# Kernel optimization log

Hardware: AMD Instinct MI355X
Metric: run time of the kernel (lower is better)

The kernel has to match this reference:

```python
import jax, jax.numpy as jnp
import numpy as np

N = 50000   # nodes
E = 1000000 # edges
D = 64      # input_dim
H = 64      # hidden dim (both hidden layers)
O = 16      # output_dim
G = 512     # number of graphs in the batch


def setup_inputs() -> dict:
    key = jax.random.key(0)
    ks = jax.random.split(key, 12)
    s = 0.05
    x = jax.random.normal(ks[0], (N, D), dtype=jnp.float32)
    edge_index = jax.random.randint(ks[1], (2, E), 0, N, dtype=jnp.int32)
    batch = jnp.sort(jax.random.randint(ks[2], (N,), 0, G, dtype=jnp.int32))
    # SAGEConv layer 1: lin_l (neighbor aggregate, with bias), lin_r (root, no bias)
    Wl1 = jax.random.normal(ks[3], (D, H), dtype=jnp.float32) * s
    Wr1 = jax.random.normal(ks[4], (D, H), dtype=jnp.float32) * s
    b1 = jnp.zeros((H,), dtype=jnp.float32)
    # SAGEConv layer 2
    Wl2 = jax.random.normal(ks[5], (H, H), dtype=jnp.float32) * s
    Wr2 = jax.random.normal(ks[6], (H, H), dtype=jnp.float32) * s
    b2 = jnp.zeros((H,), dtype=jnp.float32)
    # final Linear head
    Wo = jax.random.normal(ks[7], (H, O), dtype=jnp.float32) * s
    bo = jnp.zeros((O,), dtype=jnp.float32)
    return {"x": x, "edge_index": edge_index, "batch": batch,
            "Wl1": Wl1, "Wr1": Wr1, "b1": b1,
            "Wl2": Wl2, "Wr2": Wr2, "b2": b2,
            "Wo": Wo, "bo": bo}


def reference(x, edge_index, batch, Wl1, Wr1, b1, Wl2, Wr2, b2, Wo, bo):
    src, dst = edge_index[0], edge_index[1]  # source_to_target message flow

    def sage(h, Wl, Wr, b):
        # aggr='add': sum messages x_j from src into dst, then
        # out = lin_l(aggr) + lin_r(h)   (PyG SAGEConv, bias on lin_l)
        agg = jax.ops.segment_sum(h[src], dst, num_segments=N)  # [N, d]
        return agg @ Wl + h @ Wr + b

    h = jax.nn.relu(sage(x, Wl1, Wr1, b1))
    h = jax.nn.relu(sage(h, Wl2, Wr2, b2))
    g = jax.ops.segment_sum(h, batch, num_segments=G)  # global_add_pool -> [G, H]
    # dropout is identity in eval mode
    return g @ Wo + bo  # [G, O]
```

## Files before the change

kernel.cpp:

```cpp
#include <hip/hip_runtime.h>


namespace {
constexpr int NN = 50000;
constexpr int NE = 1000000;
constexpr int NG = 512;
constexpr int NO = 16;
constexpr int KB = 98;
constexpr int BCAP = 16000;
constexpr int EPT = 8;
constexpr int EPB = 256 * EPT;
constexpr int SBLK = (NE + EPB - 1) / EPB;
constexpr int SEDGE = 12288;
constexpr int CVT_BLK = (NN * 64 / 8 + 255) / 256;
constexpr int WP_BLK = 64;
}

typedef __attribute__((ext_vector_type(8))) short bf16x8;
typedef __attribute__((ext_vector_type(4))) float f32x4;

__device__ __forceinline__ unsigned short f2bf(float f) {
  unsigned u = __float_as_uint(f);
  u += 0x7FFFu + ((u >> 16) & 1u);
  return (unsigned short)(u >> 16);
}

__global__ __launch_bounds__(256) void prep_all(
    const float* __restrict__ x, unsigned short* __restrict__ x_bf,
    const float* __restrict__ Wl1, const float* __restrict__ Wr1,
    const float* __restrict__ Wl2, const float* __restrict__ Wr2,
    unsigned short* __restrict__ Wt1, unsigned short* __restrict__ Wt2,
    const int* __restrict__ ei, int* __restrict__ bcount,
    unsigned int* __restrict__ ebuf) {
  __shared__ unsigned int stage[EPB];
  __shared__ int cnt[128];
  __shared__ int lbase[128];
  __shared__ int cur[128];
  __shared__ int gbase[128];
  __shared__ int total_sh;
  int b = blockIdx.x;
  int t = threadIdx.x;

  if (b < CVT_BLK) {
    int i = b * 256 + t;
    if (i >= NN * 8) return;
    const float4* p = reinterpret_cast<const float4*>(x) + (size_t)i * 2;
    float4 a = p[0], bb = p[1];
    uint4 u;
    u.x = (unsigned)f2bf(a.x) | ((unsigned)f2bf(a.y) << 16);
    u.y = (unsigned)f2bf(a.z) | ((unsigned)f2bf(a.w) << 16);
    u.z = (unsigned)f2bf(bb.x) | ((unsigned)f2bf(bb.y) << 16);
    u.w = (unsigned)f2bf(bb.z) | ((unsigned)f2bf(bb.w) << 16);
    reinterpret_cast<uint4*>(x_bf)[i] = u;
    return;
  }
  if (b < CVT_BLK + WP_BLK) {
    int id = (b - CVT_BLK) * 256 + t;
    int half = id >> 13;
    int e = id & 8191;
    int nrow = e >> 7;
    int kk = e & 127;
    const float* Wl = half ? Wl2 : Wl1;
    const float* Wr = half ? Wr2 : Wr1;
    unsigned short* Wt = half ? Wt2 : Wt1;
    float v = (kk < 64) ? Wl[kk * 64 + nrow] : Wr[(kk - 64) * 64 + nrow];
    Wt[nrow * 128 + kk] = f2bf(v);
    return;
  }
  int sb = b - (CVT_BLK + WP_BLK);
  if (t < 128) cnt[t] = 0;
  __syncthreads();
  int e0 = sb * EPB;
  unsigned int pk[EPT];
#pragma unroll
  for (int i = 0; i < EPT; ++i) {
    int e = e0 + i * 256 + t;
    if (e < NE) {
      unsigned int src = (unsigned int)ei[e];
      unsigned int dst = (unsigned int)ei[NE + e];
      pk[i] = (dst << 16) | src;
      atomicAdd(&cnt[dst >> 9], 1);
    } else {
      pk[i] = 0xFFFFFFFFu;
    }
  }
  __syncthreads();
  int deg = (t < 128) ? cnt[t] : 0;
  for (int off = 1; off < 128; off <<= 1) {
    int u = (t >= off && t < 128) ? cnt[t - off] : 0;
    __syncthreads();
    if (t < 128) cnt[t] += u;
    __syncthreads();
  }
  if (t < 128) {
    int excl = cnt[t] - deg;
    lbase[t] = excl;
    cur[t] = excl;
    if (t < KB) gbase[t] = t * BCAP + atomicAdd(&bcount[t], deg);
    if (t == 127) total_sh = cnt[127];
  }
  __syncthreads();
#pragma unroll
  for (int i = 0; i < EPT; ++i) {
    if (pk[i] != 0xFFFFFFFFu) {
      int bb2 = pk[i] >> 25;
      int s = atomicAdd(&cur[bb2], 1);
      stage[s] = pk[i];
    }
  }
  __syncthreads();
  int total = total_sh;
  for (int s = t; s < total; s += 256) {
    unsigned int p = stage[s];
    int bb2 = p >> 25;
    ebuf[gbase[bb2] + (s - lbase[bb2])] = p;
  }
}

__global__ __launch_bounds__(512) void bucket_sort(
    const unsigned int* __restrict__ ebuf, const int* __restrict__ bcount,
    unsigned int* __restrict__ meta, unsigned short* __restrict__ col) {
  __shared__ unsigned int se[SEDGE];
  __shared__ int cnt[512];
  __shared__ int cur[512];
  int b = blockIdx.x;
  int t = threadIdx.x;
  int n = bcount[b];
  const unsigned int* eb = ebuf + (size_t)b * BCAP;
  cnt[t] = 0;
  __syncthreads();
  for (int j = t; j < n; j += 512) {
    unsigned int p = eb[j];
    if (j < SEDGE) se[j] = p;
    atomicAdd(&cnt[(p >> 16) & 511], 1);
  }
  __syncthreads();
  int deg = cnt[t];
  for (int off = 1; off < 512; off <<= 1) {
    int u = (t >= off) ? cnt[t - off] : 0;
    __syncthreads();
    cnt[t] += u;
    __syncthreads();
  }
  int excl = cnt[t] - deg;
  cur[t] = excl;
  int node = (b << 9) + t;
  if (node < NN) {
    meta[node] = ((unsigned)(b * BCAP + excl) << 11) | (unsigned)deg;
  }
  __syncthreads();
  unsigned short* cb = col + (size_t)b * BCAP;
  for (int j = t; j < n; j += 512) {
    unsigned int p = (j < SEDGE) ? se[j] : eb[j];
    int d = (p >> 16) & 511;
    int pos = atomicAdd(&cur[d], 1);
    cb[pos] = (unsigned short)(p & 0xFFFFu);
  }
}

template <bool POOL>
__global__ __launch_bounds__(256) void sage_fused(
    const unsigned short* __restrict__ feat,
    const unsigned int* __restrict__ meta,
    const unsigned short* __restrict__ col,
    const unsigned short* __restrict__ Wt, const float* __restrict__ bias,
    unsigned short* __restrict__ out, const int* __restrict__ batch,
    float* __restrict__ pooled) {
  __shared__ __align__(16) unsigned short tile[2][16][72];
  __shared__ float psm[POOL ? 2 : 1][16][64];
  int tid = threadIdx.x;
  int wave = tid >> 6;
  int lane = tid & 63;
  int grp = wave >> 1;
  int wv = wave & 1;
  long base = ((long)blockIdx.x * 2 + grp) * 16;

  {
    int h = lane >> 3;
    int o = lane & 7;
    long row = base + wv * 8 + h;
    int beg = 0, deg = 0;
    if (row < NN) {
      unsigned int md = meta[row];
      beg = (int)(md >> 11);
      deg = (int)(md & 2047u);
    }
    const uint4* fb = reinterpret_cast<const uint4*>(feat);
    float a0 = 0.f, a1 = 0.f, a2 = 0.f, a3 = 0.f;
    float a4 = 0.f, a5 = 0.f, a6 = 0.f, a7 = 0.f;
    for (int j = 0; j < deg; ++j) {
      int s = col[beg + j];
      uint4 u = fb[(size_t)s * 8 + o];
      a0 += __uint_as_float(u.x << 16);
      a1 += __uint_as_float(u.x & 0xFFFF0000u);
      a2 += __uint_as_float(u.y << 16);
      a3 += __uint_as_float(u.y & 0xFFFF0000u);
      a4 += __uint_as_float(u.z << 16);
      a5 += __uint_as_float(u.z & 0xFFFF0000u);
      a6 += __uint_as_float(u.w << 16);
      a7 += __uint_as_float(u.w & 0xFFFF0000u);
    }
    uint4 pk;
    pk.x = (unsigned)f2bf(a0) | ((unsigned)f2bf(a1) << 16);
    pk.y = (unsigned)f2bf(a2) | ((unsigned)f2bf(a3) << 16);
    pk.z = (unsigned)f2bf(a4) | ((unsigned)f2bf(a5) << 16);
    pk.w = (unsigned)f2bf(a6) | ((unsigned)f2bf(a7) << 16);
    *reinterpret_cast<uint4*>(&tile[grp][wv * 8 + h][o * 8]) = pk;
  }
  __syncthreads();

  int m = lane & 15;
  int q = lane >> 4;
  bool active = (base < NN);
  f32x4 acc[2];
  if (active) {
    long rowm = base + m;
    if (rowm >= NN) rowm = NN - 1;
    bf16x8 af[4];
    af[0] = *reinterpret_cast<const bf16x8*>(&tile[grp][m][q * 8]);
    af[1] = *reinterpret_cast<const bf16x8*>(&tile[grp][m][32 + q * 8]);
    const unsigned short* hrow = feat + rowm * 64;
    af[2] = *(const bf16x8*)(hrow + q * 8);
    af[3] = *(const bf16x8*)(hrow + 32 + q * 8);

#pragma unroll
    for (int tt = 0; tt < 2; ++tt) {
      int t = wv * 2 + tt;
      float bv = bias[t * 16 + m];
      acc[tt][0] = bv;
      acc[tt][1] = bv;
      acc[tt][2] = bv;
      acc[tt][3] = bv;
      const unsigned short* wrow = Wt + (size_t)(t * 16 + m) * 128 + q * 8;
#pragma unroll
      for (int s = 0; s < 4; ++s) {
        bf16x8 bfm = *(const bf16x8*)(wrow + s * 32);
        acc[tt] = __builtin_amdgcn_mfma_f32_16x16x32_bf16(af[s], bfm, acc[tt],
                                                          0, 0, 0);
      }
    }

    if (POOL) {
#pragma unroll
      for (int r = 0; r < 4; ++r) {
#pragma unroll
        for (int tt = 0; tt < 2; ++tt) {
          psm[grp][q * 4 + r][(wv * 2 + tt) * 16 + m] = fmaxf(acc[tt][r], 0.f);
        }
      }
    } else {
#pragma unroll
      for (int r = 0; r < 4; ++r) {
        long rowc = base + q * 4 + r;
        if (rowc < NN) {
          unsigned short* orow = out + rowc * 64;
#pragma unroll
          for (int tt = 0; tt < 2; ++tt) {
            orow[(wv * 2 + tt) * 16 + m] = f2bf(fmaxf(acc[tt][r], 0.f));
          }
        }
      }
    }
  }

  if (POOL) {
    __syncthreads();
    if (tid < 128) {
      int g2 = tid >> 6;
      int c = tid & 63;
      long tbase = ((long)blockIdx.x * 2 + g2) * 16;
      if (tbase < NN) {
        float run = 0.f;
        int g = batch[tbase];
        for (int i = 0; i < 16; ++i) {
          long rowi = tbase + i;
          if (rowi >= NN) break;
          int gi = batch[rowi];
          if (gi != g) {
            atomicAdd(&pooled[(size_t)g * 64 + c], run);
            run = 0.f;
            g = gi;
          }
          run += psm[g2][i][c];
        }
        atomicAdd(&pooled[(size_t)g * 64 + c], run);
      }
    }
  }
}

__global__ __launch_bounds__(256) void head_kernel(
    const float* __restrict__ pooled, const float* __restrict__ Wo,
    const float* __restrict__ bo, float* __restrict__ out) {
  int id = blockIdx.x * 256 + threadIdx.x;
  if (id >= NG * NO) return;
  int g = id >> 4, o = id & 15;
  float acc = bo[o];
  const float* p = pooled + (size_t)g * 64;
#pragma unroll
  for (int k = 0; k < 64; ++k) acc += p[k] * Wo[k * 16 + o];
  out[id] = acc;
}

extern "C" void kernel_launch(void* const* d_in, const int* in_sizes, int n_in,
                              void* d_out, int out_size, void* d_ws,
                              size_t ws_size, hipStream_t stream) {
  const float* x = (const float*)d_in[0];
  const int* ei = (const int*)d_in[1];
  const int* batch = (const int*)d_in[2];
  const float* Wl1 = (const float*)d_in[3];
  const float* Wr1 = (const float*)d_in[4];
  const float* b1 = (const float*)d_in[5];
  const float* Wl2 = (const float*)d_in[6];
  const float* Wr2 = (const float*)d_in[7];
  const float* b2 = (const float*)d_in[8];
  const float* Wo = (const float*)d_in[9];
  const float* bo = (const float*)d_in[10];
  float* out = (float*)d_out;

  unsigned short* x_bf = (unsigned short*)d_ws;
  unsigned short* h1_bf = x_bf + (size_t)NN * 64;
  unsigned short* col = h1_bf + (size_t)NN * 64;
  unsigned short* Wt1 = col + (size_t)KB * BCAP;
  unsigned short* Wt2 = Wt1 + 64 * 128;
  unsigned int* ebuf = (unsigned int*)(Wt2 + 64 * 128);
  unsigned int* meta = ebuf + (size_t)KB * BCAP;
  int* bcount = (int*)(meta + NN);
  float* pooled = (float*)(bcount + KB);

  hipMemsetAsync(bcount, 0, KB * sizeof(int) + (size_t)NG * 64 * sizeof(float),
                 stream);

  const int fused_blocks = (NN + 31) / 32;

  prep_all<<<CVT_BLK + WP_BLK + SBLK, 256, 0, stream>>>(
      x, x_bf, Wl1, Wr1, Wl2, Wr2, Wt1, Wt2, ei, bcount, ebuf);

  bucket_sort<<<KB, 512, 0, stream>>>(ebuf, bcount, meta, col);

  sage_fused<false><<<fused_blocks, 256, 0, stream>>>(
      x_bf, meta, col, Wt1, b1, h1_bf, batch, pooled);

  sage_fused<true><<<fused_blocks, 256, 0, stream>>>(
      h1_bf, meta, col, Wt2, b2, nullptr, batch, pooled);

  head_kernel<<<(NG * NO + 255) / 256, 256, 0, stream>>>(pooled, Wo, bo, out);
}
```

Before: 183.9 us.

## Split each node's edge gather across two lane halves, one 16-row tile per block

Each block now handles one 16-node tile instead of two. Each node's neighbour gather is split across two groups of 8 lanes that take alternate edges, and their partial sums are combined with a shuffle. Each wave computes a single 16-column MFMA output tile, the root-feature and bias loads are hoisted ahead of the gather, and the tail bounds checks are dropped because NN divides by 16. The aim is more memory-level parallelism in the gather-bound aggregation and more blocks in flight, at the cost of a shuffle reduction and twice as many blocks.

```diff
diff --git a/kernel.cpp b/kernel.cpp
--- a/kernel.cpp
+++ b/kernel.cpp
@@ -166,29 +166,33 @@
     const unsigned short* __restrict__ Wt, const float* __restrict__ bias,
     unsigned short* __restrict__ out, const int* __restrict__ batch,
     float* __restrict__ pooled) {
-  __shared__ __align__(16) unsigned short tile[2][16][72];
-  __shared__ float psm[POOL ? 2 : 1][16][64];
+  __shared__ __align__(16) unsigned short tile[16][72];
+  __shared__ float psm[16][64];
   int tid = threadIdx.x;
   int wave = tid >> 6;
   int lane = tid & 63;
-  int grp = wave >> 1;
-  int wv = wave & 1;
-  long base = ((long)blockIdx.x * 2 + grp) * 16;
+  long base = (long)blockIdx.x * 16;
+
+  int m = lane & 15;
+  int q = lane >> 4;
+
+  const unsigned short* hrow = feat + (base + m) * 64;
+  bf16x8 af2 = *(const bf16x8*)(hrow + q * 8);
+  bf16x8 af3 = *(const bf16x8*)(hrow + 32 + q * 8);
+  float bv = bias[wave * 16 + m];
 
   {
-    int h = lane >> 3;
+    int r = lane >> 4;
+    int h = (lane >> 3) & 1;
     int o = lane & 7;
-    long row = base + wv * 8 + h;
-    int beg = 0, deg = 0;
-    if (row < NN) {
-      unsigned int md = meta[row];
-      beg = (int)(md >> 11);
-      deg = (int)(md & 2047u);
-    }
+    long row = base + wave * 4 + r;
+    unsigned int md = meta[row];
+    int beg = (int)(md >> 11);
+    int deg = (int)(md & 2047u);
     const uint4* fb = reinterpret_cast<const uint4*>(feat);
     float a0 = 0.f, a1 = 0.f, a2 = 0.f, a3 = 0.f;
     float a4 = 0.f, a5 = 0.f, a6 = 0.f, a7 = 0.f;
-    for (int j = 0; j < deg; ++j) {
+    for (int j = h; j < deg; j += 2) {
       int s = col[beg + j];
       uint4 u = fb[(size_t)s * 8 + o];
       a0 += __uint_as_float(u.x << 16);
@@ -200,91 +204,68 @@
       a6 += __uint_as_float(u.w << 16);
       a7 += __uint_as_float(u.w & 0xFFFF0000u);
     }
-    uint4 pk;
-    pk.x = (unsigned)f2bf(a0) | ((unsigned)f2bf(a1) << 16);
-    pk.y = (unsigned)f2bf(a2) | ((unsigned)f2bf(a3) << 16);
-    pk.z = (unsigned)f2bf(a4) | ((unsigned)f2bf(a5) << 16);
-    pk.w = (unsigned)f2bf(a6) | ((unsigned)f2bf(a7) << 16);
-    *reinterpret_cast<uint4*>(&tile[grp][wv * 8 + h][o * 8]) = pk;
-  }
-  __syncthreads();
-
-  int m = lane & 15;
-  int q = lane >> 4;
-  bool active = (base < NN);
-  f32x4 acc[2];
-  if (active) {
-    long rowm = base + m;
-    if (rowm >= NN) rowm = NN - 1;
-    bf16x8 af[4];
-    af[0] = *reinterpret_cast<const bf16x8*>(&tile[grp][m][q * 8]);
-    af[1] = *reinterpret_cast<const bf16x8*>(&tile[grp][m][32 + q * 8]);
-    const unsigned short* hrow = feat + rowm * 64;
-    af[2] = *(const bf16x8*)(hrow + q * 8);
-    af[3] = *(const bf16x8*)(hrow + 32 + q * 8);
-
-#pragma unroll
-    for (int tt = 0; tt < 2; ++tt) {
-      int t = wv * 2 + tt;
-      float bv = bias[t * 16 + m];
-      acc[tt][0] = bv;
-      acc[tt][1] = bv;
-      acc[tt][2] = bv;
-      acc[tt][3] = bv;
-      const unsigned short* wrow = Wt + (size_t)(t * 16 + m) * 128 + q * 8;
-#pragma unroll
-      for (int s = 0; s < 4; ++s) {
-        bf16x8 bfm = *(const bf16x8*)(wrow + s * 32);
-        acc[tt] = __builtin_amdgcn_mfma_f32_16x16x32_bf16(af[s], bfm, acc[tt],
-                                                          0, 0, 0);
+    a0 += __shfl_xor(a0, 8);
+    a1 += __shfl_xor(a1, 8);
+    a2 += __shfl_xor(a2, 8);
+    a3 += __shfl_xor(a3, 8);
+    a4 += __shfl_xor(a4, 8);
+    a5 += __shfl_xor(a5, 8);
+    a6 += __shfl_xor(a6, 8);
+    a7 += __shfl_xor(a7, 8);
+    if (h == 0) {
+      uint4 pk;
+      pk.x = (unsigned)f2bf(a0) | ((unsigned)f2bf(a1) << 16);
+      pk.y = (unsigned)f2bf(a2) | ((unsigned)f2bf(a3) << 16);
+      pk.z = (unsigned)f2bf(a4) | ((unsigned)f2bf(a5) << 16);
+      pk.w = (unsigned)f2bf(a6) | ((unsigned)f2bf(a7) << 16);
+      *reinterpret_cast<uint4*>(&tile[wave * 4 + r][o * 8]) = pk;
+    }
+  }
+  __syncthreads();
+
+  bf16x8 af0 = *reinterpret_cast<const bf16x8*>(&tile[m][q * 8]);
+  bf16x8 af1 = *reinterpret_cast<const bf16x8*>(&tile[m][32 + q * 8]);
+  f32x4 acc;
+  acc[0] = bv;
+  acc[1] = bv;
+  acc[2] = bv;
+  acc[3] = bv;
+  const unsigned short* wrow = Wt + (size_t)(wave * 16 + m) * 128 + q * 8;
+  acc = __builtin_amdgcn_mfma_f32_16x16x32_bf16(
+      af0, *(const bf16x8*)(wrow + 0), acc, 0, 0, 0);
+  acc = __builtin_amdgcn_mfma_f32_16x16x32_bf16(
+      af1, *(const bf16x8*)(wrow + 32), acc, 0, 0, 0);
+  acc = __builtin_amdgcn_mfma_f32_16x16x32_bf16(
+      af2, *(const bf16x8*)(wrow + 64), acc, 0, 0, 0);
+  acc = __builtin_amdgcn_mfma_f32_16x16x32_bf16(
+      af3, *(const bf16x8*)(wrow + 96), acc, 0, 0, 0);
+
+  if (POOL) {
+#pragma unroll
+    for (int r2 = 0; r2 < 4; ++r2) {
+      psm[q * 4 + r2][wave * 16 + m] = fmaxf(acc[r2], 0.f);
+    }
+    __syncthreads();
+    if (tid < 64) {
+      int c = tid;
+      float run = 0.f;
+      int g = batch[base];
+      for (int i = 0; i < 16; ++i) {
+        int gi = batch[base + i];
+        if (gi != g) {
+          atomicAdd(&pooled[(size_t)g * 64 + c], run);
+          run = 0.f;
+          g = gi;
+        }
+        run += psm[i][c];
       }
-    }
-
-    if (POOL) {
-#pragma unroll
-      for (int r = 0; r < 4; ++r) {
-#pragma unroll
-        for (int tt = 0; tt < 2; ++tt) {
-          psm[grp][q * 4 + r][(wv * 2 + tt) * 16 + m] = fmaxf(acc[tt][r], 0.f);
-        }
-      }
-    } else {
-#pragma unroll
-      for (int r = 0; r < 4; ++r) {
-        long rowc = base + q * 4 + r;
-        if (rowc < NN) {
-          unsigned short* orow = out + rowc * 64;
-#pragma unroll
-          for (int tt = 0; tt < 2; ++tt) {
-            orow[(wv * 2 + tt) * 16 + m] = f2bf(fmaxf(acc[tt][r], 0.f));
-          }
-        }
-      }
-    }
-  }
-
-  if (POOL) {
-    __syncthreads();
-    if (tid < 128) {
-      int g2 = tid >> 6;
-      int c = tid & 63;
-      long tbase = ((long)blockIdx.x * 2 + g2) * 16;
-      if (tbase < NN) {
-        float run = 0.f;
-        int g = batch[tbase];
-        for (int i = 0; i < 16; ++i) {
-          long rowi = tbase + i;
-          if (rowi >= NN) break;
-          int gi = batch[rowi];
-          if (gi != g) {
-            atomicAdd(&pooled[(size_t)g * 64 + c], run);
-            run = 0.f;
-            g = gi;
-          }
-          run += psm[g2][i][c];
-        }
-        atomicAdd(&pooled[(size_t)g * 64 + c], run);
-      }
+      atomicAdd(&pooled[(size_t)g * 64 + c], run);
+    }
+  } else {
+#pragma unroll
+    for (int r2 = 0; r2 < 4; ++r2) {
+      unsigned short* orow = out + (base + q * 4 + r2) * 64;
+      orow[wave * 16 + m] = f2bf(fmaxf(acc[r2], 0.f));
     }
   }
 }
@@ -331,7 +312,7 @@
   hipMemsetAsync(bcount, 0, KB * sizeof(int) + (size_t)NG * 64 * sizeof(float),
                  stream);
 
-  const int fused_blocks = (NN + 31) / 32;
+  const int fused_blocks = NN / 16;
 
   prep_all<<<CVT_BLK + WP_BLK + SBLK, 256, 0, stream>>>(
       x, x_bf, Wl1, Wr1, Wl2, Wr2, Wt1, Wt2, ei, bcount, ebuf);
```

After: 180.2 us. 2.0% less time.
